# Performance work log

Hardware: AMD Instinct MI355X
Metric: run time of the kernel (lower is better)

## Reference

```python
import jax, jax.numpy as jnp
import numpy as np

H, F, E = 1024, 2816, 8   # hidden_size, intermediate_size, num_local_experts
B, S = 2, 2048
TOP_K = 2


def setup_inputs() -> dict:
    key = jax.random.key(0)
    ks = jax.random.split(key, 5)
    scale = 0.02
    return {
        "hidden_states": jax.random.normal(ks[0], (B, S, H), jnp.float32),
        "gate_w": jax.random.normal(ks[1], (E, H), jnp.float32) * scale,
        "w1": jax.random.normal(ks[2], (E, F, H), jnp.float32) * scale,
        "w3": jax.random.normal(ks[3], (E, F, H), jnp.float32) * scale,
        "w2": jax.random.normal(ks[4], (E, H, F), jnp.float32) * scale,
    }


def reference(hidden_states, gate_w, w1, w3, w2):
    b, s, h = hidden_states.shape
    e = gate_w.shape[0]
    T = b * s
    x = hidden_states.reshape(T, h)                      # [T, H]
    router_logits = x @ gate_w.T                         # [T, E]
    probs = jax.nn.softmax(router_logits, axis=-1)
    topw, sel = jax.lax.top_k(probs, TOP_K)              # [T, K]
    topw = topw / jnp.sum(topw, axis=-1, keepdims=True)  # renormalize over top-k
    # dense combine weights [T, E] (equivalent to the per-expert scatter/index_add)
    comb = jnp.zeros((T, e), x.dtype).at[jnp.arange(T)[:, None], sel].add(topw)
    hidden = jax.nn.silu(jnp.einsum('th,efh->etf', x, w1)) * jnp.einsum('th,efh->etf', x, w3)
    y = jnp.einsum('etf,ehf->eth', hidden, w2)           # [E, T, H]
    out = jnp.einsum('eth,te->th', y, comb)              # weighted scatter-combine
    return out.reshape(b, s, h), router_logits
```

## Files before the change

### kernel.cpp

```cpp
#include <hip/hip_runtime.h>
#include <hip/hip_bf16.h>
#include <stdint.h>

#define T_TOK 4096
#define H_DIM 1024
#define F_DIM 2816
#define E_NUM 8

typedef __attribute__((ext_vector_type(8))) __bf16 bf16x8;
typedef __attribute__((ext_vector_type(4))) float floatx4;
typedef __attribute__((address_space(3))) char lds_char;
typedef __attribute__((address_space(1))) const char glb_char;

__device__ __forceinline__ void gload16(const void* g, void* l) {
  __builtin_amdgcn_global_load_lds((glb_char*)g, (lds_char*)l, 16, 0, 0);
}

__device__ __forceinline__ unsigned pack2bf16(float a, float b) {
  unsigned ua = __builtin_bit_cast(unsigned, a);
  unsigned ub = __builtin_bit_cast(unsigned, b);
  ua += 0x7fffu + ((ua >> 16) & 1u);
  ub += 0x7fffu + ((ub >> 16) & 1u);
  return (ua >> 16) | (ub & 0xffff0000u);
}

__device__ __forceinline__ float b2f(unsigned short u) {
  unsigned v = ((unsigned)u) << 16;
  return __builtin_bit_cast(float, v);
}

__device__ __forceinline__ int swz(int row, int colb) {
  return (row * 128 + colb) ^ ((row & 7) << 4);
}

__global__ __launch_bounds__(256) void convert_kernel(
    const float* __restrict__ src, __hip_bfloat16* __restrict__ dst,
    int nchunk8) {
  int i = blockIdx.x * blockDim.x + threadIdx.x;
  const int stride = gridDim.x * blockDim.x;
  for (; i < nchunk8; i += stride) {
    const float4* s = (const float4*)(src + (size_t)i * 8);
    float4 a = s[0], b = s[1];
    uint4 p;
    p.x = pack2bf16(a.x, a.y); p.y = pack2bf16(a.z, a.w);
    p.z = pack2bf16(b.x, b.y); p.w = pack2bf16(b.z, b.w);
    *(uint4*)((char*)dst + (size_t)i * 16) = p;
  }
}

__global__ __launch_bounds__(256) void convert_w13(
    const float* __restrict__ w1, const float* __restrict__ w3,
    __hip_bfloat16* __restrict__ wB) {
  const int e = blockIdx.y;
  const int rho = blockIdx.x * 2 + (threadIdx.x >> 7);
  const int hc = threadIdx.x & 127;
  const int f = ((rho >> 5) << 4) + (rho & 15);
  const float* src = ((rho >> 4) & 1 ? w3 : w1) +
                     ((size_t)e * F_DIM + f) * H_DIM + hc * 8;
  const float4* s = (const float4*)src;
  float4 a = s[0], b = s[1];
  uint4 p;
  p.x = pack2bf16(a.x, a.y); p.y = pack2bf16(a.z, a.w);
  p.z = pack2bf16(b.x, b.y); p.w = pack2bf16(b.z, b.w);
  *(uint4*)((char*)wB + (((size_t)e * (2 * F_DIM) + rho) * H_DIM + hc * 8) * 2)
      = p;
}

__global__ __launch_bounds__(256) void router_kernel(
    const float* __restrict__ x, const float* __restrict__ gate,
    float* __restrict__ logits_out, __hip_bfloat16* __restrict__ xb,
    int* __restrict__ counts, int* __restrict__ idx_list,
    float* __restrict__ wgt_list, int* __restrict__ meta0,
    int* __restrict__ meta1, float* __restrict__ wcomb)
{
  const int wv = threadIdx.x >> 6;
  const int lane = threadIdx.x & 63;
  const int t = blockIdx.x * 4 + wv;

  const float4* xr = (const float4*)(x + (size_t)t * H_DIM);
  const float4* g4 = (const float4*)gate;

  float acc[E_NUM];
#pragma unroll
  for (int e = 0; e < E_NUM; ++e) acc[e] = 0.f;

  unsigned* xbo = (unsigned*)(xb + (size_t)t * H_DIM);
#pragma unroll
  for (int j = 0; j < 4; ++j) {
    int i = j * 64 + lane;
    float4 xv = xr[i];
    uint2 pk;
    pk.x = pack2bf16(xv.x, xv.y);
    pk.y = pack2bf16(xv.z, xv.w);
    *(uint2*)(xbo + i * 2) = pk;
#pragma unroll
    for (int e = 0; e < E_NUM; ++e) {
      float4 gv = g4[e * 256 + i];
      acc[e] += xv.x * gv.x + xv.y * gv.y + xv.z * gv.z + xv.w * gv.w;
    }
  }
#pragma unroll
  for (int off = 32; off > 0; off >>= 1) {
#pragma unroll
    for (int e = 0; e < E_NUM; ++e) acc[e] += __shfl_xor(acc[e], off, 64);
  }

  if (lane == 0) {
#pragma unroll
    for (int e = 0; e < E_NUM; ++e) logits_out[(size_t)t * E_NUM + e] = acc[e];
    int i0 = 0; float v0 = acc[0];
#pragma unroll
    for (int e = 1; e < E_NUM; ++e) if (acc[e] > v0) { v0 = acc[e]; i0 = e; }
    int i1 = -1; float v1 = -1e30f;
#pragma unroll
    for (int e = 0; e < E_NUM; ++e)
      if (e != i0 && acc[e] > v1) { v1 = acc[e]; i1 = e; }
    float p1 = __expf(v1 - v0);
    float w0 = 1.f / (1.f + p1);
    float w1 = p1 / (1.f + p1);
    int pos0 = atomicAdd(&counts[i0], 1);
    idx_list[i0 * T_TOK + pos0] = t;
    wgt_list[i0 * T_TOK + pos0] = w0;
    int pos1 = atomicAdd(&counts[i1], 1);
    idx_list[i1 * T_TOK + pos1] = t;
    wgt_list[i1 * T_TOK + pos1] = w1;
    meta0[t] = (i0 << 16) | pos0;
    meta1[t] = (i1 << 16) | pos1;
    wcomb[t] = w0;
  }
}

__global__ void scan_kernel(const int* __restrict__ counts,
                            int* __restrict__ offsets) {
  if (threadIdx.x == 0) {
    int s = 0;
    for (int e = 0; e < E_NUM; ++e) { offsets[e] = s; s += counts[e]; }
  }
}

__global__ __launch_bounds__(512, 2) void gemm1_kernel(
    const __hip_bfloat16* __restrict__ xb,
    const __hip_bfloat16* __restrict__ wB,
    const int* __restrict__ counts, const int* __restrict__ offsets,
    const int* __restrict__ idx_list, __hip_bfloat16* __restrict__ hidden)
{
  const int L = blockIdx.x + 22 * (blockIdx.y + 16 * blockIdx.z);
  const int k = L & 7;
  const int r = L >> 3;
  const int tn = r >> 4;
  const int tm = r & 15;
  const int e = (k - tn) & 7;
  const int n_e = counts[e];
  if (n_e == 0 || tm * 256 >= n_e) return;
  const int off_e = offsets[e];

  __shared__ char lds[131072];
  char* sA = lds;
  char* sB = lds + 65536;

  const int tid = threadIdx.x;
  const int lane = tid & 63;
  const int wv = tid >> 6;
  const int wrow = (wv >> 2) * 128;
  const int wcol = (wv & 3) * 64;
  const int csw = ((lane & 7) ^ (lane >> 3)) << 4;
  const int wvb = wv * 1024;

  size_t aoff[4];
#pragma unroll
  for (int i = 0; i < 4; ++i) {
    int rr = i * 64 + wv * 8 + (lane >> 3);
    int pos = tm * 256 + rr;
    int p = pos < n_e ? pos : n_e - 1;
    aoff[i] = (size_t)idx_list[e * T_TOK + p] * 2048;
  }
  const char* xbp = (const char*)xb;
  const char* wBp =
      (const char*)wB + ((size_t)e * (2 * F_DIM) + tn * 256) * 2048;
  size_t boff[4];
#pragma unroll
  for (int i = 0; i < 4; ++i)
    boff[i] = (size_t)(i * 64 + wv * 8 + (lane >> 3)) * 2048;

  floatx4 acc[8][4];
#pragma unroll
  for (int m = 0; m < 8; ++m)
#pragma unroll
    for (int n = 0; n < 4; ++n)
#pragma unroll
      for (int q = 0; q < 4; ++q) acc[m][n][q] = 0.f;

#define STAGE1(set, kb)                                                \
  do {                                                                 \
    char* dA = sA + (set) * 32768 + wvb;                               \
    char* dB = sB + (set) * 32768 + wvb;                               \
    _Pragma("unroll")                                                  \
    for (int i = 0; i < 4; ++i) {                                      \
      gload16(xbp + aoff[i] + (kb) + csw, dA + i * 8192);              \
      gload16(wBp + boff[i] + (kb) + csw, dB + i * 8192);              \
    }                                                                  \
  } while (0)

  asm volatile("s_waitcnt vmcnt(0)" ::: "memory");
  STAGE1(0, 0);

  int cur = 0;
  for (int kt = 0; kt < H_DIM / 64; ++kt) {
    if (kt < H_DIM / 64 - 1) {
      STAGE1(cur ^ 1, (kt + 1) * 128);
      asm volatile("s_waitcnt vmcnt(8)" ::: "memory");
    } else {
      asm volatile("s_waitcnt vmcnt(0)" ::: "memory");
    }
    __syncthreads();
    const char* rA = sA + cur * 32768;
    const char* rB = sB + cur * 32768;
#pragma unroll
    for (int kk = 0; kk < 2; ++kk) {
      const int colb = kk * 64 + (lane >> 4) * 16;
      bf16x8 af[8], bx[4];
#pragma unroll
      for (int m = 0; m < 8; ++m)
        af[m] = *(const bf16x8*)(rA + swz(wrow + m * 16 + (lane & 15), colb));
#pragma unroll
      for (int n = 0; n < 4; ++n)
        bx[n] = *(const bf16x8*)(rB + swz(wcol + n * 16 + (lane & 15), colb));
#pragma unroll
      for (int m = 0; m < 8; ++m)
#pragma unroll
        for (int n = 0; n < 4; ++n)
          acc[m][n] = __builtin_amdgcn_mfma_f32_16x16x32_bf16(
              af[m], bx[n], acc[m][n], 0, 0, 0);
    }
    __syncthreads();
    cur ^= 1;
  }
#undef STAGE1

  const int fbase = (tn * 8 + (wcol >> 5)) * 16 + (lane & 15);
#pragma unroll
  for (int m = 0; m < 8; ++m) {
#pragma unroll
    for (int q = 0; q < 4; ++q) {
      int pos = tm * 256 + wrow + m * 16 + ((lane >> 4) << 2) + q;
      if (pos < n_e) {
        __hip_bfloat16* hrow = hidden + (size_t)(off_e + pos) * F_DIM;
#pragma unroll
        for (int j = 0; j < 2; ++j) {
          float h1 = acc[m][2 * j][q];
          float h3 = acc[m][2 * j + 1][q];
          float h = (h1 / (1.f + __expf(-h1))) * h3;
          hrow[fbase + j * 16] = __float2bfloat16(h);
        }
      }
    }
  }
}

__global__ __launch_bounds__(256, 2) void gemm2_kernel(
    const __hip_bfloat16* __restrict__ hidden,
    const __hip_bfloat16* __restrict__ w2b,
    const int* __restrict__ counts, const int* __restrict__ offsets,
    __hip_bfloat16* __restrict__ y)
{
  const int e = blockIdx.z & 7;
  const int kh = blockIdx.z >> 3;
  const int tm = blockIdx.y;
  const int tn = blockIdx.x;
  const int n_e = counts[e];
  if (n_e == 0 || tm * 128 >= n_e) return;
  const int n0 = tn * 128;
  const int off_e = offsets[e];
  const int kbase = kh * (F_DIM);

  __shared__ char lds[65536];
  char* sA = lds;
  char* sB = lds + 32768;

  const int tid = threadIdx.x;
  const int lane = tid & 63;
  const int wv = tid >> 6;
  const int wrow = (wv >> 1) * 64;
  const int wcol = (wv & 1) * 64;
  const int csw = ((lane & 7) ^ (lane >> 3)) << 4;
  const int wvb = wv * 1024;

  size_t aoff[4], boff[4];
#pragma unroll
  for (int i = 0; i < 4; ++i) {
    int rr = i * 32 + wv * 8 + (lane >> 3);
    int pos = tm * 128 + rr;
    int p = pos < n_e ? pos : n_e - 1;
    aoff[i] = (size_t)(off_e + p) * (F_DIM * 2);
    boff[i] = ((size_t)e * H_DIM + n0 + rr) * (F_DIM * 2);
  }
  const char* hp = (const char*)hidden;
  const char* w2p = (const char*)w2b;

  floatx4 acc[4][4];
#pragma unroll
  for (int m = 0; m < 4; ++m)
#pragma unroll
    for (int n = 0; n < 4; ++n)
#pragma unroll
      for (int q = 0; q < 4; ++q) acc[m][n][q] = 0.f;

#define STAGE2(set, kb)                                                \
  do {                                                                 \
    char* dA = sA + (set) * 16384 + wvb;                               \
    char* dB = sB + (set) * 16384 + wvb;                               \
    _Pragma("unroll")                                                  \
    for (int i = 0; i < 4; ++i) {                                      \
      gload16(hp + aoff[i] + (kb) + csw, dA + i * 4096);               \
      gload16(w2p + boff[i] + (kb) + csw, dB + i * 4096);              \
    }                                                                  \
  } while (0)

  asm volatile("s_waitcnt vmcnt(0)" ::: "memory");
  STAGE2(0, kbase);

  int cur = 0;
  const int NKT = F_DIM / 64 / 2;
  for (int kt = 0; kt < NKT; ++kt) {
    if (kt < NKT - 1) {
      STAGE2(cur ^ 1, kbase + (kt + 1) * 128);
      asm volatile("s_waitcnt vmcnt(8)" ::: "memory");
    } else {
      asm volatile("s_waitcnt vmcnt(0)" ::: "memory");
    }
    __syncthreads();
    const char* rA = sA + cur * 16384;
    const char* rB = sB + cur * 16384;
#pragma unroll
    for (int kk = 0; kk < 2; ++kk) {
      const int colb = kk * 64 + (lane >> 4) * 16;
      bf16x8 af[4], bx[4];
#pragma unroll
      for (int m = 0; m < 4; ++m)
        af[m] = *(const bf16x8*)(rA + swz(wrow + m * 16 + (lane & 15), colb));
#pragma unroll
      for (int n = 0; n < 4; ++n)
        bx[n] = *(const bf16x8*)(rB + swz(wcol + n * 16 + (lane & 15), colb));
#pragma unroll
      for (int m = 0; m < 4; ++m)
#pragma unroll
        for (int n = 0; n < 4; ++n)
          acc[m][n] = __builtin_amdgcn_mfma_f32_16x16x32_bf16(
              af[m], bx[n], acc[m][n], 0, 0, 0);
    }
    __syncthreads();
    cur ^= 1;
  }
#undef STAGE2

  __hip_bfloat16* yh = y + (size_t)kh * (2 * T_TOK) * H_DIM;
#pragma unroll
  for (int m = 0; m < 4; ++m) {
#pragma unroll
    for (int q = 0; q < 4; ++q) {
      int pos = tm * 128 + wrow + m * 16 + ((lane >> 4) << 2) + q;
      if (pos < n_e) {
        __hip_bfloat16* yrow = yh + (size_t)(off_e + pos) * H_DIM + n0;
#pragma unroll
        for (int n = 0; n < 4; ++n)
          yrow[wcol + n * 16 + (lane & 15)] = __float2bfloat16(acc[m][n][q]);
      }
    }
  }
}

__global__ __launch_bounds__(256) void combine_kernel(
    const __hip_bfloat16* __restrict__ y, const int* __restrict__ offsets,
    const int* __restrict__ meta0, const int* __restrict__ meta1,
    const float* __restrict__ wcomb, float* __restrict__ out)
{
  const int t = blockIdx.x;
  const int m0 = meta0[t], m1 = meta1[t];
  const float w0 = wcomb[t];
  const float w1 = 1.f - w0;
  const size_t s0 = (size_t)(offsets[m0 >> 16] + (m0 & 0xffff)) * H_DIM;
  const size_t s1 = (size_t)(offsets[m1 >> 16] + (m1 & 0xffff)) * H_DIM;
  const size_t HB = (size_t)(2 * T_TOK) * H_DIM;
  const int c = threadIdx.x * 4;
  ushort4 a0 = *(const ushort4*)(y + s0 + c);
  ushort4 a1 = *(const ushort4*)(y + HB + s0 + c);
  ushort4 b0 = *(const ushort4*)(y + s1 + c);
  ushort4 b1 = *(const ushort4*)(y + HB + s1 + c);
  float4 o;
  o.x = w0 * (b2f(a0.x) + b2f(a1.x)) + w1 * (b2f(b0.x) + b2f(b1.x));
  o.y = w0 * (b2f(a0.y) + b2f(a1.y)) + w1 * (b2f(b0.y) + b2f(b1.y));
  o.z = w0 * (b2f(a0.z) + b2f(a1.z)) + w1 * (b2f(b0.z) + b2f(b1.z));
  o.w = w0 * (b2f(a0.w) + b2f(a1.w)) + w1 * (b2f(b0.w) + b2f(b1.w));
  *(float4*)(out + (size_t)t * H_DIM + c) = o;
}

__global__ __launch_bounds__(256) void gemm1_fb(
    const __hip_bfloat16* __restrict__ xb,
    const float* __restrict__ w1, const float* __restrict__ w3,
    const int* __restrict__ counts, const int* __restrict__ offsets,
    const int* __restrict__ idx_list, __hip_bfloat16* __restrict__ hidden)
{
  const int e = blockIdx.z;
  const int n_e = counts[e];
  const int tm = blockIdx.y;
  if (n_e == 0 || tm * 128 >= n_e) return;
  const int tn = blockIdx.x;
  const int f0 = tn * 128;
  const int off_e = offsets[e];

  __shared__ short sA[128 * 64];
  __shared__ short sB1[128 * 64];
  __shared__ short sB3[128 * 64];
  __shared__ int s_row[128];

  const int tid = threadIdx.x;
  if (tid < 128) {
    int pos = tm * 128 + tid;
    int p = pos < n_e ? pos : n_e - 1;
    s_row[tid] = idx_list[e * T_TOK + p];
  }
  const int lane = tid & 63;
  const int wv = tid >> 6;
  const int wrow = (wv >> 1) * 64;
  const int wcol = (wv & 1) * 64;
  const int cc = tid & 7;
  const int rbase = tid >> 3;

  floatx4 acc1[4][4], acc3[4][4];
#pragma unroll
  for (int m = 0; m < 4; ++m)
#pragma unroll
    for (int n = 0; n < 4; ++n)
#pragma unroll
      for (int q = 0; q < 4; ++q) { acc1[m][n][q] = 0.f; acc3[m][n][q] = 0.f; }

  const float* w1e = w1 + (size_t)e * F_DIM * H_DIM + (size_t)f0 * H_DIM;
  const float* w3e = w3 + (size_t)e * F_DIM * H_DIM + (size_t)f0 * H_DIM;

  for (int kt = 0; kt < H_DIM / 64; ++kt) {
    const int k0 = kt * 64;
    __syncthreads();
#pragma unroll
    for (int i = 0; i < 4; ++i) {
      int rr = rbase + 32 * i;
      uint4 av = *(const uint4*)(xb + (size_t)s_row[rr] * H_DIM + k0 + cc * 8);
      *(uint4*)((char*)sA + swz(rr, cc * 16)) = av;
      const float4* p1 = (const float4*)(w1e + (size_t)rr * H_DIM + k0 + cc * 8);
      float4 a1 = p1[0], b1 = p1[1];
      uint4 pb1;
      pb1.x = pack2bf16(a1.x, a1.y); pb1.y = pack2bf16(a1.z, a1.w);
      pb1.z = pack2bf16(b1.x, b1.y); pb1.w = pack2bf16(b1.z, b1.w);
      *(uint4*)((char*)sB1 + swz(rr, cc * 16)) = pb1;
      const float4* p3 = (const float4*)(w3e + (size_t)rr * H_DIM + k0 + cc * 8);
      float4 a3 = p3[0], b3 = p3[1];
      uint4 pb3;
      pb3.x = pack2bf16(a3.x, a3.y); pb3.y = pack2bf16(a3.z, a3.w);
      pb3.z = pack2bf16(b3.x, b3.y); pb3.w = pack2bf16(b3.z, b3.w);
      *(uint4*)((char*)sB3 + swz(rr, cc * 16)) = pb3;
    }
    __syncthreads();
#pragma unroll
    for (int kk = 0; kk < 2; ++kk) {
      const int colb = kk * 64 + (lane >> 4) * 16;
      bf16x8 af[4], bf1[4], bf3[4];
#pragma unroll
      for (int m = 0; m < 4; ++m)
        af[m] = *(const bf16x8*)((const char*)sA +
                                 swz(wrow + m * 16 + (lane & 15), colb));
#pragma unroll
      for (int n = 0; n < 4; ++n) {
        bf1[n] = *(const bf16x8*)((const char*)sB1 +
                                  swz(wcol + n * 16 + (lane & 15), colb));
        bf3[n] = *(const bf16x8*)((const char*)sB3 +
                                  swz(wcol + n * 16 + (lane & 15), colb));
      }
#pragma unroll
      for (int m = 0; m < 4; ++m)
#pragma unroll
        for (int n = 0; n < 4; ++n) {
          acc1[m][n] = __builtin_amdgcn_mfma_f32_16x16x32_bf16(
              af[m], bf1[n], acc1[m][n], 0, 0, 0);
          acc3[m][n] = __builtin_amdgcn_mfma_f32_16x16x32_bf16(
              af[m], bf3[n], acc3[m][n], 0, 0, 0);
        }
    }
  }
#pragma unroll
  for (int m = 0; m < 4; ++m) {
#pragma unroll
    for (int q = 0; q < 4; ++q) {
      int rl = wrow + m * 16 + ((lane >> 4) << 2) + q;
      int pos = tm * 128 + rl;
      if (pos < n_e) {
        __hip_bfloat16* hrow = hidden + (size_t)(off_e + pos) * F_DIM + f0;
#pragma unroll
        for (int n = 0; n < 4; ++n) {
          float h1 = acc1[m][n][q];
          float h3 = acc3[m][n][q];
          float h = (h1 / (1.f + __expf(-h1))) * h3;
          hrow[wcol + n * 16 + (lane & 15)] = __float2bfloat16(h);
        }
      }
    }
  }
}

__global__ __launch_bounds__(256) void gemm2_fb(
    const __hip_bfloat16* __restrict__ hidden, const float* __restrict__ w2,
    const int* __restrict__ counts, const int* __restrict__ offsets,
    const int* __restrict__ idx_list, const float* __restrict__ wgt_list,
    float* __restrict__ out)
{
  const int e = blockIdx.z;
  const int n_e = counts[e];
  const int tm = blockIdx.y;
  if (n_e == 0 || tm * 128 >= n_e) return;
  const int tn = blockIdx.x;
  const int n0 = tn * 128;
  const int off_e = offsets[e];

  __shared__ short sA[128 * 64];
  __shared__ short sB[128 * 64];
  __shared__ int s_tok[128];
  __shared__ float s_wgt[128];

  const int tid = threadIdx.x;
  if (tid < 128) {
    int pos = tm * 128 + tid;
    if (pos < n_e) {
      s_tok[tid] = idx_list[e * T_TOK + pos];
      s_wgt[tid] = wgt_list[e * T_TOK + pos];
    } else {
      s_tok[tid] = -1;
      s_wgt[tid] = 0.f;
    }
  }
  const int lane = tid & 63;
  const int wv = tid >> 6;
  const int wrow = (wv >> 1) * 64;
  const int wcol = (wv & 1) * 64;
  const int cc = tid & 7;
  const int rbase = tid >> 3;

  floatx4 acc[4][4];
#pragma unroll
  for (int m = 0; m < 4; ++m)
#pragma unroll
    for (int n = 0; n < 4; ++n)
#pragma unroll
      for (int q = 0; q < 4; ++q) acc[m][n][q] = 0.f;

  const float* w2e = w2 + (size_t)e * H_DIM * F_DIM + (size_t)n0 * F_DIM;

  for (int kt = 0; kt < F_DIM / 64; ++kt) {
    const int k0 = kt * 64;
    __syncthreads();
#pragma unroll
    for (int i = 0; i < 4; ++i) {
      int rr = rbase + 32 * i;
      int pos = tm * 128 + rr;
      int pr = pos < n_e ? pos : n_e - 1;
      uint4 av = *(const uint4*)(hidden + (size_t)(off_e + pr) * F_DIM +
                                 k0 + cc * 8);
      *(uint4*)((char*)sA + swz(rr, cc * 16)) = av;
      const float4* pb = (const float4*)(w2e + (size_t)rr * F_DIM + k0 + cc * 8);
      float4 ba = pb[0], bb = pb[1];
      uint4 pk;
      pk.x = pack2bf16(ba.x, ba.y); pk.y = pack2bf16(ba.z, ba.w);
      pk.z = pack2bf16(bb.x, bb.y); pk.w = pack2bf16(bb.z, bb.w);
      *(uint4*)((char*)sB + swz(rr, cc * 16)) = pk;
    }
    __syncthreads();
#pragma unroll
    for (int kk = 0; kk < 2; ++kk) {
      const int colb = kk * 64 + (lane >> 4) * 16;
      bf16x8 af[4], bf[4];
#pragma unroll
      for (int m = 0; m < 4; ++m)
        af[m] = *(const bf16x8*)((const char*)sA +
                                 swz(wrow + m * 16 + (lane & 15), colb));
#pragma unroll
      for (int n = 0; n < 4; ++n)
        bf[n] = *(const bf16x8*)((const char*)sB +
                                 swz(wcol + n * 16 + (lane & 15), colb));
#pragma unroll
      for (int m = 0; m < 4; ++m)
#pragma unroll
        for (int n = 0; n < 4; ++n)
          acc[m][n] = __builtin_amdgcn_mfma_f32_16x16x32_bf16(
              af[m], bf[n], acc[m][n], 0, 0, 0);
    }
  }
#pragma unroll
  for (int m = 0; m < 4; ++m) {
#pragma unroll
    for (int q = 0; q < 4; ++q) {
      int rl = wrow + m * 16 + ((lane >> 4) << 2) + q;
      int tok = s_tok[rl];
      if (tok >= 0) {
        float wgt = s_wgt[rl];
        float* orow = out + (size_t)tok * H_DIM + n0;
#pragma unroll
        for (int n = 0; n < 4; ++n)
          atomicAdd(&orow[wcol + n * 16 + (lane & 15)], wgt * acc[m][n][q]);
      }
    }
  }
}

extern "C" void kernel_launch(void* const* d_in, const int* in_sizes, int n_in,
                              void* d_out, int out_size, void* d_ws,
                              size_t ws_size, hipStream_t stream) {
  const float* x = (const float*)d_in[0];
  const float* gate = (const float*)d_in[1];
  const float* w1 = (const float*)d_in[2];
  const float* w3 = (const float*)d_in[3];
  const float* w2 = (const float*)d_in[4];

  float* out = (float*)d_out;
  float* logits = out + (size_t)T_TOK * H_DIM;

  char* ws = (char*)d_ws;
  const size_t o_idx = 256;
  const size_t o_wgt = o_idx + (size_t)E_NUM * T_TOK * 4;
  const size_t o_m0  = o_wgt + (size_t)E_NUM * T_TOK * 4;
  const size_t o_m1  = o_m0 + (size_t)T_TOK * 4;
  const size_t o_wc  = o_m1 + (size_t)T_TOK * 4;
  const size_t o_xb  = o_wc + (size_t)T_TOK * 4;
  const size_t o_hid = o_xb + (size_t)T_TOK * H_DIM * 2;
  const size_t o_wB  = o_hid + (size_t)2 * T_TOK * F_DIM * 2;
  const size_t o_w2b = o_wB + (size_t)E_NUM * 2 * F_DIM * H_DIM * 2;
  const size_t need  = o_w2b + (size_t)E_NUM * H_DIM * F_DIM * 2;

  int* counts = (int*)ws;
  int* offsets = counts + 8;
  int* idx_list = (int*)(ws + o_idx);
  float* wgt_list = (float*)(ws + o_wgt);
  int* meta0 = (int*)(ws + o_m0);
  int* meta1 = (int*)(ws + o_m1);
  float* wcomb = (float*)(ws + o_wc);
  __hip_bfloat16* xb = (__hip_bfloat16*)(ws + o_xb);
  __hip_bfloat16* hidden = (__hip_bfloat16*)(ws + o_hid);

  hipMemsetAsync(counts, 0, 64, stream);

  if (ws_size >= need) {
    __hip_bfloat16* wB = (__hip_bfloat16*)(ws + o_wB);
    __hip_bfloat16* w2b = (__hip_bfloat16*)(ws + o_w2b);
    __hip_bfloat16* y = (__hip_bfloat16*)(ws + o_wB);

    convert_w13<<<dim3(F_DIM, E_NUM), 256, 0, stream>>>(w1, w3, wB);
    convert_kernel<<<2048, 256, 0, stream>>>(
        w2, w2b, E_NUM * F_DIM * H_DIM / 8);
    router_kernel<<<T_TOK / 4, 256, 0, stream>>>(
        x, gate, logits, xb, counts, idx_list, wgt_list, meta0, meta1, wcomb);
    scan_kernel<<<1, 64, 0, stream>>>(counts, offsets);
    gemm1_kernel<<<dim3(22, 16, E_NUM), 512, 0, stream>>>(
        xb, wB, counts, offsets, idx_list, hidden);
    gemm2_kernel<<<dim3(8, 32, 2 * E_NUM), 256, 0, stream>>>(
        hidden, w2b, counts, offsets, y);
    combine_kernel<<<T_TOK, 256, 0, stream>>>(y, offsets, meta0, meta1, wcomb,
                                              out);
  } else {
    hipMemsetAsync(out, 0, (size_t)T_TOK * H_DIM * sizeof(float), stream);
    router_kernel<<<T_TOK / 4, 256, 0, stream>>>(
        x, gate, logits, xb, counts, idx_list, wgt_list, meta0, meta1, wcomb);
    scan_kernel<<<1, 64, 0, stream>>>(counts, offsets);
    gemm1_fb<<<dim3(F_DIM / 128, T_TOK / 128, E_NUM), 256, 0, stream>>>(
        xb, w1, w3, counts, offsets, idx_list, hidden);
    gemm2_fb<<<dim3(H_DIM / 128, T_TOK / 128, E_NUM), 256, 0, stream>>>(
        hidden, w2, counts, offsets, idx_list, wgt_list, out);
  }
}
```

Baseline: 447.2 us.

## Drop LDS double buffering in expert GEMMs to raise occupancy

```diff
diff --git a/kernel.cpp b/kernel.cpp
--- a/kernel.cpp
+++ b/kernel.cpp
@@ -138,7 +138,7 @@
   }
 }
 
-__global__ __launch_bounds__(512, 2) void gemm1_kernel(
+__global__ __launch_bounds__(512, 4) void gemm1_kernel(
     const __hip_bfloat16* __restrict__ xb,
     const __hip_bfloat16* __restrict__ wB,
     const int* __restrict__ counts, const int* __restrict__ offsets,
@@ -154,9 +154,9 @@
   if (n_e == 0 || tm * 256 >= n_e) return;
   const int off_e = offsets[e];
 
-  __shared__ char lds[131072];
+  __shared__ char lds[65536];
   char* sA = lds;
-  char* sB = lds + 65536;
+  char* sB = lds + 32768;
 
   const int tid = threadIdx.x;
   const int lane = tid & 63;
@@ -190,41 +190,26 @@
 #pragma unroll
       for (int q = 0; q < 4; ++q) acc[m][n][q] = 0.f;
 
-#define STAGE1(set, kb)                                                \
-  do {                                                                 \
-    char* dA = sA + (set) * 32768 + wvb;                               \
-    char* dB = sB + (set) * 32768 + wvb;                               \
-    _Pragma("unroll")                                                  \
-    for (int i = 0; i < 4; ++i) {                                      \
-      gload16(xbp + aoff[i] + (kb) + csw, dA + i * 8192);              \
-      gload16(wBp + boff[i] + (kb) + csw, dB + i * 8192);              \
-    }                                                                  \
-  } while (0)
-
-  asm volatile("s_waitcnt vmcnt(0)" ::: "memory");
-  STAGE1(0, 0);
-
-  int cur = 0;
   for (int kt = 0; kt < H_DIM / 64; ++kt) {
-    if (kt < H_DIM / 64 - 1) {
-      STAGE1(cur ^ 1, (kt + 1) * 128);
-      asm volatile("s_waitcnt vmcnt(8)" ::: "memory");
-    } else {
-      asm volatile("s_waitcnt vmcnt(0)" ::: "memory");
-    }
+    const int kb = kt * 128;
+    if (kt > 0) __syncthreads();
+#pragma unroll
+    for (int i = 0; i < 4; ++i) {
+      gload16(xbp + aoff[i] + kb + csw, sA + wvb + i * 8192);
+      gload16(wBp + boff[i] + kb + csw, sB + wvb + i * 8192);
+    }
+    asm volatile("s_waitcnt vmcnt(0)" ::: "memory");
     __syncthreads();
-    const char* rA = sA + cur * 32768;
-    const char* rB = sB + cur * 32768;
 #pragma unroll
     for (int kk = 0; kk < 2; ++kk) {
       const int colb = kk * 64 + (lane >> 4) * 16;
       bf16x8 af[8], bx[4];
 #pragma unroll
       for (int m = 0; m < 8; ++m)
-        af[m] = *(const bf16x8*)(rA + swz(wrow + m * 16 + (lane & 15), colb));
+        af[m] = *(const bf16x8*)(sA + swz(wrow + m * 16 + (lane & 15), colb));
 #pragma unroll
       for (int n = 0; n < 4; ++n)
-        bx[n] = *(const bf16x8*)(rB + swz(wcol + n * 16 + (lane & 15), colb));
+        bx[n] = *(const bf16x8*)(sB + swz(wcol + n * 16 + (lane & 15), colb));
 #pragma unroll
       for (int m = 0; m < 8; ++m)
 #pragma unroll
@@ -232,10 +217,7 @@
           acc[m][n] = __builtin_amdgcn_mfma_f32_16x16x32_bf16(
               af[m], bx[n], acc[m][n], 0, 0, 0);
     }
-    __syncthreads();
-    cur ^= 1;
-  }
-#undef STAGE1
+  }
 
   const int fbase = (tn * 8 + (wcol >> 5)) * 16 + (lane & 15);
 #pragma unroll
@@ -257,7 +239,7 @@
   }
 }
 
-__global__ __launch_bounds__(256, 2) void gemm2_kernel(
+__global__ __launch_bounds__(256, 4) void gemm2_kernel(
     const __hip_bfloat16* __restrict__ hidden,
     const __hip_bfloat16* __restrict__ w2b,
     const int* __restrict__ counts, const int* __restrict__ offsets,
@@ -273,9 +255,9 @@
   const int off_e = offsets[e];
   const int kbase = kh * (F_DIM);
 
-  __shared__ char lds[65536];
+  __shared__ char lds[32768];
   char* sA = lds;
-  char* sB = lds + 32768;
+  char* sB = lds + 16384;
 
   const int tid = threadIdx.x;
   const int lane = tid & 63;
@@ -305,42 +287,27 @@
 #pragma unroll
       for (int q = 0; q < 4; ++q) acc[m][n][q] = 0.f;
 
-#define STAGE2(set, kb)                                                \
-  do {                                                                 \
-    char* dA = sA + (set) * 16384 + wvb;                               \
-    char* dB = sB + (set) * 16384 + wvb;                               \
-    _Pragma("unroll")                                                  \
-    for (int i = 0; i < 4; ++i) {                                      \
-      gload16(hp + aoff[i] + (kb) + csw, dA + i * 4096);               \
-      gload16(w2p + boff[i] + (kb) + csw, dB + i * 4096);              \
-    }                                                                  \
-  } while (0)
-
-  asm volatile("s_waitcnt vmcnt(0)" ::: "memory");
-  STAGE2(0, kbase);
-
-  int cur = 0;
   const int NKT = F_DIM / 64 / 2;
   for (int kt = 0; kt < NKT; ++kt) {
-    if (kt < NKT - 1) {
-      STAGE2(cur ^ 1, kbase + (kt + 1) * 128);
-      asm volatile("s_waitcnt vmcnt(8)" ::: "memory");
-    } else {
-      asm volatile("s_waitcnt vmcnt(0)" ::: "memory");
-    }
+    const int kb = kbase + kt * 128;
+    if (kt > 0) __syncthreads();
+#pragma unroll
+    for (int i = 0; i < 4; ++i) {
+      gload16(hp + aoff[i] + kb + csw, sA + wvb + i * 4096);
+      gload16(w2p + boff[i] + kb + csw, sB + wvb + i * 4096);
+    }
+    asm volatile("s_waitcnt vmcnt(0)" ::: "memory");
     __syncthreads();
-    const char* rA = sA + cur * 16384;
-    const char* rB = sB + cur * 16384;
 #pragma unroll
     for (int kk = 0; kk < 2; ++kk) {
       const int colb = kk * 64 + (lane >> 4) * 16;
       bf16x8 af[4], bx[4];
 #pragma unroll
       for (int m = 0; m < 4; ++m)
-        af[m] = *(const bf16x8*)(rA + swz(wrow + m * 16 + (lane & 15), colb));
+        af[m] = *(const bf16x8*)(sA + swz(wrow + m * 16 + (lane & 15), colb));
 #pragma unroll
       for (int n = 0; n < 4; ++n)
-        bx[n] = *(const bf16x8*)(rB + swz(wcol + n * 16 + (lane & 15), colb));
+        bx[n] = *(const bf16x8*)(sB + swz(wcol + n * 16 + (lane & 15), colb));
 #pragma unroll
       for (int m = 0; m < 4; ++m)
 #pragma unroll
@@ -348,10 +315,7 @@
           acc[m][n] = __builtin_amdgcn_mfma_f32_16x16x32_bf16(
               af[m], bx[n], acc[m][n], 0, 0, 0);
     }
-    __syncthreads();
-    cur ^= 1;
-  }
-#undef STAGE2
+  }
 
   __hip_bfloat16* yh = y + (size_t)kh * (2 * T_TOK) * H_DIM;
 #pragma unroll
```

Measured after the change: 1.151 ms. +157.3%, slower.

## Interleave prefetch loads with MFMA phases in stage-1 GEMM loop

Applied to the files above, without the earlier changes.

```diff
diff --git a/kernel.cpp b/kernel.cpp
--- a/kernel.cpp
+++ b/kernel.cpp
@@ -190,52 +190,67 @@
 #pragma unroll
       for (int q = 0; q < 4; ++q) acc[m][n][q] = 0.f;
 
-#define STAGE1(set, kb)                                                \
+#define STAGE1_PART(set, kb, i)                                        \
   do {                                                                 \
     char* dA = sA + (set) * 32768 + wvb;                               \
     char* dB = sB + (set) * 32768 + wvb;                               \
-    _Pragma("unroll")                                                  \
-    for (int i = 0; i < 4; ++i) {                                      \
-      gload16(xbp + aoff[i] + (kb) + csw, dA + i * 8192);              \
-      gload16(wBp + boff[i] + (kb) + csw, dB + i * 8192);              \
-    }                                                                  \
+    gload16(xbp + aoff[i] + (kb) + csw, dA + (i) * 8192);              \
+    gload16(wBp + boff[i] + (kb) + csw, dB + (i) * 8192);              \
   } while (0)
 
   asm volatile("s_waitcnt vmcnt(0)" ::: "memory");
-  STAGE1(0, 0);
-
-  int cur = 0;
+#pragma unroll
+  for (int i = 0; i < 4; ++i) STAGE1_PART(0, 0, i);
+
   for (int kt = 0; kt < H_DIM / 64; ++kt) {
-    if (kt < H_DIM / 64 - 1) {
-      STAGE1(cur ^ 1, (kt + 1) * 128);
-      asm volatile("s_waitcnt vmcnt(8)" ::: "memory");
-    } else {
-      asm volatile("s_waitcnt vmcnt(0)" ::: "memory");
-    }
-    __syncthreads();
+    const int cur = kt & 1;
     const char* rA = sA + cur * 32768;
     const char* rB = sB + cur * 32768;
-#pragma unroll
-    for (int kk = 0; kk < 2; ++kk) {
+    const bool pre = kt < H_DIM / 64 - 1;
+    const int nkb = (kt + 1) * 128;
+#pragma unroll
+    for (int p = 0; p < 4; ++p) {
+      const int mh = p >> 1;
+      const int kk = p & 1;
       const int colb = kk * 64 + (lane >> 4) * 16;
-      bf16x8 af[8], bx[4];
-#pragma unroll
-      for (int m = 0; m < 8; ++m)
-        af[m] = *(const bf16x8*)(rA + swz(wrow + m * 16 + (lane & 15), colb));
-#pragma unroll
-      for (int n = 0; n < 4; ++n)
-        bx[n] = *(const bf16x8*)(rB + swz(wcol + n * 16 + (lane & 15), colb));
-#pragma unroll
-      for (int m = 0; m < 8; ++m)
+      bf16x8 af[4], bx[4];
+      if (p == 0) {
+        if (pre) STAGE1_PART(cur ^ 1, nkb, 0);
+        if (pre) asm volatile("s_waitcnt vmcnt(2)" ::: "memory");
+        else     asm volatile("s_waitcnt vmcnt(0)" ::: "memory");
+        __syncthreads();
+#pragma unroll
+        for (int i = 0; i < 4; ++i)
+          af[i] = *(const bf16x8*)(rA +
+                       swz(wrow + (mh * 4 + i) * 16 + (lane & 15), colb));
 #pragma unroll
         for (int n = 0; n < 4; ++n)
-          acc[m][n] = __builtin_amdgcn_mfma_f32_16x16x32_bf16(
-              af[m], bx[n], acc[m][n], 0, 0, 0);
-    }
-    __syncthreads();
-    cur ^= 1;
-  }
-#undef STAGE1
+          bx[n] = *(const bf16x8*)(rB +
+                       swz(wcol + n * 16 + (lane & 15), colb));
+      } else {
+#pragma unroll
+        for (int i = 0; i < 4; ++i)
+          af[i] = *(const bf16x8*)(rA +
+                       swz(wrow + (mh * 4 + i) * 16 + (lane & 15), colb));
+#pragma unroll
+        for (int n = 0; n < 4; ++n)
+          bx[n] = *(const bf16x8*)(rB +
+                       swz(wcol + n * 16 + (lane & 15), colb));
+        if (pre) STAGE1_PART(cur ^ 1, nkb, p);
+        __syncthreads();
+      }
+      __builtin_amdgcn_s_setprio(1);
+#pragma unroll
+      for (int i = 0; i < 4; ++i)
+#pragma unroll
+        for (int n = 0; n < 4; ++n)
+          acc[mh * 4 + i][n] = __builtin_amdgcn_mfma_f32_16x16x32_bf16(
+              af[i], bx[n], acc[mh * 4 + i][n], 0, 0, 0);
+      __builtin_amdgcn_s_setprio(0);
+      __syncthreads();
+    }
+  }
+#undef STAGE1_PART
 
   const int fbase = (tn * 8 + (wcol >> 5)) * 16 + (lane & 15);
 #pragma unroll
```

Result: slower. 531.2 us (+18.8%).
